# Optimization experiments

Hardware: AMD Instinct MI355X
Metric: run time of the kernel (lower is better)

Reference implementation:

```python
import jax, jax.numpy as jnp
import numpy as np

B, S, D, H = 2, 2048, 1024, 16
HD = D // H          # 64
NREF = HD // 2       # 32 Householder reflections
BLOCK = 128          # flex_attention block granularity
ROPE_BASE = 10000.0


def setup_inputs() -> dict:
    key = jax.random.key(0)
    ks = jax.random.split(key, 12)
    x = jax.random.normal(ks[0], (B, S, D), jnp.float32)
    # block-causal block mask (flex_attention block_mask analogue)
    nb = S // BLOCK
    bm = jnp.tril(jnp.ones((nb, nb), bool))
    mask = jnp.repeat(jnp.repeat(bm, BLOCK, axis=0), BLOCK, axis=1)  # [S,S]
    s = lambda fan: fan ** -0.5
    vs = jax.random.normal(ks[1], (NREF, HD), jnp.float32) * 0.02
    w_qkv = jax.random.normal(ks[2], (D, 3 * D), jnp.float32) * s(D)
    w_out = jax.random.normal(ks[3], (D, D), jnp.float32) * s(D)
    w_gate = jax.random.normal(ks[4], (D, D), jnp.float32) * s(D)
    b_gate = jnp.zeros((D,), jnp.float32)
    w_mlp_gate = jax.random.normal(ks[5], (D, 8 * D), jnp.float32) * s(D)
    b_mlp_gate = jnp.zeros((8 * D,), jnp.float32)
    w_mlp_out = jax.random.normal(ks[6], (4 * D, D), jnp.float32) * s(4 * D)
    b_mlp_out = jnp.zeros((D,), jnp.float32)
    return dict(x=x, mask=mask, grid_size=S, vs=vs, w_qkv=w_qkv, w_out=w_out,
                w_gate=w_gate, b_gate=b_gate, w_mlp_gate=w_mlp_gate,
                b_mlp_gate=b_mlp_gate, w_mlp_out=w_mlp_out, b_mlp_out=b_mlp_out)


def rmsnorm(x):
    return x * jax.lax.rsqrt(jnp.mean(x * x, axis=-1, keepdims=True) + 1e-6)


def householder_matrix(vs):
    # Q = prod_i (I - 2 v_i v_i^T / |v_i|^2), applied sequentially as in torch loop
    def body(Q, v):
        vn = jnp.sum(v * v) + 1e-8
        return Q - (2.0 / vn) * jnp.outer(v, v @ Q), None
    Q0 = jnp.eye(HD, dtype=vs.dtype)
    Q, _ = jax.lax.scan(body, Q0, vs)
    return Q


def rope_tables(seq_len, dtype):
    inv_freq = 1.0 / (ROPE_BASE ** (jnp.arange(0, HD, 2, dtype=jnp.float32) / HD))
    ang = jnp.arange(seq_len, dtype=jnp.float32)[:, None] * inv_freq  # [S, HD/2]
    ang = jnp.concatenate([ang, ang], axis=-1)                        # [S, HD]
    return jnp.cos(ang).astype(dtype), jnp.sin(ang).astype(dtype)


def rotate_half(x):
    x1, x2 = jnp.split(x, 2, axis=-1)
    return jnp.concatenate([-x2, x1], axis=-1)


def reference(x, mask, grid_size, vs, w_qkv, w_out, w_gate, b_gate,
              w_mlp_gate, b_mlp_gate, w_mlp_out, b_mlp_out):
    del grid_size  # positions derived from sequence length
    resid = x
    h = rmsnorm(x)
    qkv = h @ w_qkv                                # [B,S,3D]
    q, k, v = jnp.split(qkv, 3, axis=-1)
    to_heads = lambda t: t.reshape(B, S, H, HD).transpose(0, 2, 1, 3)  # [B,H,S,hd]
    q, k, v = to_heads(q), to_heads(k), to_heads(v)

    # RnRoPE: inverse Householder rotation, rope, forward Householder rotation
    Q = householder_matrix(vs)                     # [hd,hd]
    q = q @ Q.T
    k = k @ Q.T
    cos, sin = rope_tables(S, x.dtype)             # [S,hd]
    cos = cos[None, None]; sin = sin[None, None]
    q = q * cos + rotate_half(q) * sin
    k = k * cos + rotate_half(k) * sin
    q = q @ Q
    k = k @ Q

    # block-sparse attention (mask realized as boolean [S,S])
    scores = jnp.einsum('bhqd,bhkd->bhqk', q, k) / jnp.sqrt(jnp.asarray(HD, x.dtype))
    scores = jnp.where(mask[None, None], scores, jnp.asarray(-1e30, x.dtype))
    attn = jnp.einsum('bhqk,bhkd->bhqd', jax.nn.softmax(scores, axis=-1), v)
    attn = attn.transpose(0, 2, 1, 3).reshape(B, S, D)
    attn = attn @ w_out

    gate = jax.nn.sigmoid(attn @ w_gate + b_gate)
    x = resid + attn * gate

    resid = x
    gv = rmsnorm(x) @ w_mlp_gate + b_mlp_gate      # [B,S,8D]
    g, val = jnp.split(gv, 2, axis=-1)
    x = resid + (val * jax.nn.gelu(g, approximate=False)) @ w_mlp_out + b_mlp_out
    return x
```

## Files before the change

kernel.cpp:

```cpp
#include <hip/hip_runtime.h>
#include <hip/hip_bf16.h>
#include <math.h>

#define BT 2
#define SEQ 2048
#define DIM 1024
#define NH 16
#define HD 64
#define NTOK (BT*SEQ)

typedef __attribute__((ext_vector_type(4))) float floatx4;
typedef __attribute__((ext_vector_type(8))) short shortx8;
typedef __attribute__((ext_vector_type(4))) short shortx4;

#define GLL16(gp, lp) __builtin_amdgcn_global_load_lds( \
    (const __attribute__((address_space(1))) unsigned int*)(const void*)(gp), \
    (__attribute__((address_space(3))) unsigned int*)(void*)(lp), 16, 0, 0)

__device__ __forceinline__ float bf2f(unsigned short u) {
    unsigned int x = ((unsigned int)u) << 16;
    return __builtin_bit_cast(float, x);
}
__device__ __forceinline__ unsigned short f2bf(float f) {
    unsigned int x = __builtin_bit_cast(unsigned int, f);
    unsigned int lsb = (x >> 16) & 1u;
    x += 0x7fffu + lsb;
    return (unsigned short)(x >> 16);
}
__device__ __forceinline__ float ldin_f(const void* p, size_t i, int isbf) {
    return isbf ? bf2f(((const unsigned short*)p)[i]) : ((const float*)p)[i];
}

__global__ void detect_kernel(const unsigned short* __restrict__ x, int* __restrict__ flag) {
    __shared__ int cnt;
    if (threadIdx.x == 0) cnt = 0;
    __syncthreads();
    unsigned short u = x[(size_t)threadIdx.x * 2];
    int e = (u >> 7) & 0xFF;
    if (e >= 100 && e <= 140) atomicAdd(&cnt, 1);
    __syncthreads();
    if (threadIdx.x == 0) *flag = (cnt >= 192) ? 1 : 0;
}

__global__ void transpose_any(const void* __restrict__ in,
                              unsigned short* __restrict__ out, int R, int C,
                              const int* __restrict__ flagp) {
    int isbf = *flagp;
    __shared__ unsigned short tile[32][33];
    int c0 = blockIdx.x * 32, r0 = blockIdx.y * 32;
    int tx = threadIdx.x, ty = threadIdx.y;
#pragma unroll
    for (int i = 0; i < 4; i++) {
        size_t idx = (size_t)(r0 + ty + i * 8) * C + c0 + tx;
        tile[ty + i * 8][tx] = isbf ? ((const unsigned short*)in)[idx]
                                    : f2bf(((const float*)in)[idx]);
    }
    __syncthreads();
#pragma unroll
    for (int i = 0; i < 4; i++)
        out[(size_t)(c0 + ty + i * 8) * R + r0 + tx] = tile[tx][ty + i * 8];
}

__global__ __launch_bounds__(64) void householder_kernel(const void* __restrict__ vs,
                                                         float* __restrict__ Qg,
                                                         const int* __restrict__ flagp) {
    int isbf = *flagp;
    __shared__ float vsh[64];
    int j = threadIdx.x;
    float Qc[64];
#pragma unroll
    for (int i = 0; i < 64; i++) Qc[i] = (i == j) ? 1.f : 0.f;
    for (int r = 0; r < 32; r++) {
        vsh[j] = ldin_f(vs, r * 64 + j, isbf);
        __syncthreads();
        float va[64];
#pragma unroll
        for (int i = 0; i < 64; i++) va[i] = vsh[i];
        float vn0 = 0.f, vn1 = 0.f, vn2 = 0.f, vn3 = 0.f;
        float t0 = 0.f, t1 = 0.f, t2 = 0.f, t3 = 0.f;
#pragma unroll
        for (int i = 0; i < 16; i++) {
            vn0 += va[4 * i + 0] * va[4 * i + 0];
            vn1 += va[4 * i + 1] * va[4 * i + 1];
            vn2 += va[4 * i + 2] * va[4 * i + 2];
            vn3 += va[4 * i + 3] * va[4 * i + 3];
            t0 += va[4 * i + 0] * Qc[4 * i + 0];
            t1 += va[4 * i + 1] * Qc[4 * i + 1];
            t2 += va[4 * i + 2] * Qc[4 * i + 2];
            t3 += va[4 * i + 3] * Qc[4 * i + 3];
        }
        float vn = (vn0 + vn1) + (vn2 + vn3) + 1e-8f;
        float t = (t0 + t1) + (t2 + t3);
        float c = (2.f / vn) * t;
#pragma unroll
        for (int i = 0; i < 64; i++) Qc[i] -= c * va[i];
        __syncthreads();
    }
#pragma unroll
    for (int i = 0; i < 64; i++) Qg[i * 64 + j] = Qc[i];
}

__global__ __launch_bounds__(256) void rotate_wqkv(unsigned short* __restrict__ wT,
                                                   const float* __restrict__ Qg) {
    __shared__ float Qs[64][64];
    __shared__ unsigned short tile[64][128];
    int bid = blockIdx.x;
    int row0 = (bid >> 3) * 64;
    int col0 = (bid & 7) * 128;
    int t = threadIdx.x;
#pragma unroll
    for (int i = 0; i < 16; i++) {
        int idx = i * 256 + t;
        Qs[idx >> 6][idx & 63] = Qg[idx];
    }
#pragma unroll
    for (int i = 0; i < 8; i++) {
        int e = i * 256 + t;
        int r = e >> 5, cg = (e & 31) * 4;
        *(shortx4*)&tile[r][cg] = *(const shortx4*)&wT[(size_t)(row0 + r) * 1024 + col0 + cg];
    }
    __syncthreads();
    int ib = t >> 5;
    int c = (t & 31) * 4;
    float acc[8][4];
#pragma unroll
    for (int rr = 0; rr < 8; rr++)
#pragma unroll
        for (int cx = 0; cx < 4; cx++) acc[rr][cx] = 0.f;
    for (int j = 0; j < 64; j++) {
        float t0 = bf2f(tile[j][c]);
        float t1 = bf2f(tile[j][c + 1]);
        float t2 = bf2f(tile[j][c + 2]);
        float t3 = bf2f(tile[j][c + 3]);
#pragma unroll
        for (int rr = 0; rr < 8; rr++) {
            float qv = Qs[rr * 8 + ib][j];
            acc[rr][0] += qv * t0;
            acc[rr][1] += qv * t1;
            acc[rr][2] += qv * t2;
            acc[rr][3] += qv * t3;
        }
    }
#pragma unroll
    for (int rr = 0; rr < 8; rr++) {
        int i = rr * 8 + ib;
        shortx4 o4;
#pragma unroll
        for (int cx = 0; cx < 4; cx++) o4[cx] = (short)f2bf(acc[rr][cx]);
        *(shortx4*)&wT[(size_t)(row0 + i) * 1024 + col0 + c] = o4;
    }
}

__global__ void rope_table(float* __restrict__ tab) {
    int idx = blockIdx.x * 256 + threadIdx.x;
    int s = idx >> 5, fi = idx & 31;
    float invf = __expf(-(float)fi * (9.210340371976184f / 32.f));
    float ang = (float)s * invf;
    tab[2 * idx]     = cosf(ang);
    tab[2 * idx + 1] = sinf(ang);
}

__global__ __launch_bounds__(256) void rmsnorm2(const void* __restrict__ x,
                                                unsigned short* __restrict__ h,
                                                const int* __restrict__ flagp) {
    int isbf = flagp ? *flagp : 1;
    __shared__ float red[256];
    int row = blockIdx.x, t = threadIdx.x;
    size_t base = (size_t)row * DIM;
    float v[4];
    float ss = 0.f;
#pragma unroll
    for (int i = 0; i < 4; i++) {
        v[i] = ldin_f(x, base + t + 256 * i, isbf);
        ss += v[i] * v[i];
    }
    red[t] = ss;
    __syncthreads();
    for (int s = 128; s > 0; s >>= 1) {
        if (t < s) red[t] += red[t + s];
        __syncthreads();
    }
    float rs = rsqrtf(red[0] * (1.f / 1024.f) + 1e-6f);
#pragma unroll
    for (int i = 0; i < 4; i++) h[base + t + 256 * i] = f2bf(v[i] * rs);
}

template<int BN, int MODE>
__global__ __launch_bounds__(256) void gemm_bt(const unsigned short* __restrict__ A,
                                               const unsigned short* __restrict__ Bt,
                                               void* __restrict__ C,
                                               const void* __restrict__ bias,
                                               const unsigned short* __restrict__ resid,
                                               const void* __restrict__ xin,
                                               const int* __restrict__ flagp,
                                               int M, int N, int K) {
    constexpr int NJ = BN / 32;
    __shared__ __align__(16) unsigned short As[2][128][32];
    __shared__ __align__(16) unsigned short Bs[2][BN][32];
    int isbf = flagp ? *flagp : 1;
    int tile = (blockIdx.x & 7) * (gridDim.x >> 3) + (blockIdx.x >> 3);
    int nbn = N / BN;
    int m0 = (tile / nbn) * 128;
    int n0 = (tile % nbn) * BN;
    int t = threadIdx.x;
    int lane = t & 63;
    int w = t >> 6;
    int wr = (w >> 1) * 64;
    int wc = (w & 1) * (16 * NJ);
    int lr = lane & 15;
    int kg = lane >> 4;

    floatx4 acc[4][NJ];
#pragma unroll
    for (int i = 0; i < 4; i++)
#pragma unroll
        for (int j = 0; j < NJ; j++) acc[i][j] = (floatx4){0.f, 0.f, 0.f, 0.f};

    int srow = w * 16 + (lane >> 2);
    int skseg = (lane & 3) * 8;
    const unsigned short* aP = A + (size_t)(m0 + srow) * K + skseg;
    const unsigned short* bP = Bt + (size_t)(n0 + srow) * K + skseg;
    size_t r64 = (size_t)64 * K;

    auto STAGE = [&](int s, int b) {
        int off = s * 32;
        GLL16(aP + off,       &As[b][w * 16][0]);
        GLL16(aP + r64 + off, &As[b][64 + w * 16][0]);
        GLL16(bP + off,       &Bs[b][w * 16][0]);
        if constexpr (BN == 128) GLL16(bP + r64 + off, &Bs[b][64 + w * 16][0]);
    };

    int NS = K / 32;
    STAGE(0, 0);
    __syncthreads();

    int cur = 0;
    for (int s = 0; s < NS; ++s) {
        if (s + 1 < NS) STAGE(s + 1, cur ^ 1);
        shortx8 af[4], bfv[NJ];
#pragma unroll
        for (int i = 0; i < 4; i++) af[i] = *(const shortx8*)&As[cur][wr + i * 16 + lr][kg * 8];
#pragma unroll
        for (int j = 0; j < NJ; j++) bfv[j] = *(const shortx8*)&Bs[cur][wc + j * 16 + lr][kg * 8];
#pragma unroll
        for (int i = 0; i < 4; i++)
#pragma unroll
            for (int j = 0; j < NJ; j++)
                acc[i][j] = __builtin_amdgcn_mfma_f32_16x16x32_bf16(af[i], bfv[j], acc[i][j], 0, 0, 0);
        __syncthreads();
        cur ^= 1;
    }
#pragma unroll
    for (int i = 0; i < 4; i++) {
#pragma unroll
        for (int j = 0; j < NJ; j++) {
            int col = n0 + wc + j * 16 + lr;
            int rbase = m0 + wr + i * 16 + kg * 4;
            float bv = bias ? ldin_f(bias, col, isbf) : 0.f;
#pragma unroll
            for (int r = 0; r < 4; r++) {
                float val = acc[i][j][r] + bv;
                size_t oidx = (size_t)(rbase + r) * N + col;
                if constexpr (MODE == 0) {
                    ((unsigned short*)C)[oidx] = f2bf(val);
                } else if constexpr (MODE == 1) {
                    ((float*)C)[oidx] = val + bf2f(resid[oidx]);
                } else {
                    float a = bf2f(resid[oidx]);
                    float sg = 1.f / (1.f + __expf(-val));
                    ((unsigned short*)C)[oidx] = f2bf(ldin_f(xin, oidx, isbf) + a * sg);
                }
            }
        }
    }
}

__global__ __launch_bounds__(256) void gemm_glu(const unsigned short* __restrict__ A,
                                                const unsigned short* __restrict__ Bt,
                                                unsigned short* __restrict__ act,
                                                const void* __restrict__ bias,
                                                const int* __restrict__ flagp) {
    __shared__ __align__(16) unsigned short As[2][128][32];
    __shared__ __align__(16) unsigned short Bg[2][64][32];
    __shared__ __align__(16) unsigned short Bv[2][64][32];
    const int K = 1024;
    int isbf = *flagp;
    int tile = (blockIdx.x & 7) * (gridDim.x >> 3) + (blockIdx.x >> 3);
    int m0 = (tile & 31) * 128;
    int n0 = (tile >> 5) * 64;
    int t = threadIdx.x;
    int lane = t & 63;
    int w = t >> 6;
    int wr = (w >> 1) * 64;
    int wc = (w & 1) * 32;
    int lr = lane & 15;
    int kg = lane >> 4;

    floatx4 ag[4][2], av[4][2];
#pragma unroll
    for (int i = 0; i < 4; i++)
#pragma unroll
        for (int j = 0; j < 2; j++) {
            ag[i][j] = (floatx4){0.f, 0.f, 0.f, 0.f};
            av[i][j] = (floatx4){0.f, 0.f, 0.f, 0.f};
        }

    int srow = w * 16 + (lane >> 2);
    int skseg = (lane & 3) * 8;
    const unsigned short* aP  = A + (size_t)(m0 + srow) * K + skseg;
    const unsigned short* bgP = Bt + (size_t)(n0 + srow) * K + skseg;
    const unsigned short* bvP = Bt + (size_t)(4096 + n0 + srow) * K + skseg;
    size_t r64 = (size_t)64 * K;

    auto STAGE = [&](int s, int b) {
        int off = s * 32;
        GLL16(aP + off,       &As[b][w * 16][0]);
        GLL16(aP + r64 + off, &As[b][64 + w * 16][0]);
        GLL16(bgP + off,      &Bg[b][w * 16][0]);
        GLL16(bvP + off,      &Bv[b][w * 16][0]);
    };

    const int NS = K / 32;
    STAGE(0, 0);
    __syncthreads();

    int cur = 0;
    for (int s = 0; s < NS; ++s) {
        if (s + 1 < NS) STAGE(s + 1, cur ^ 1);
        shortx8 af[4], gf[2], vf[2];
#pragma unroll
        for (int i = 0; i < 4; i++) af[i] = *(const shortx8*)&As[cur][wr + i * 16 + lr][kg * 8];
#pragma unroll
        for (int j = 0; j < 2; j++) {
            gf[j] = *(const shortx8*)&Bg[cur][wc + j * 16 + lr][kg * 8];
            vf[j] = *(const shortx8*)&Bv[cur][wc + j * 16 + lr][kg * 8];
        }
#pragma unroll
        for (int i = 0; i < 4; i++)
#pragma unroll
            for (int j = 0; j < 2; j++) {
                ag[i][j] = __builtin_amdgcn_mfma_f32_16x16x32_bf16(af[i], gf[j], ag[i][j], 0, 0, 0);
                av[i][j] = __builtin_amdgcn_mfma_f32_16x16x32_bf16(af[i], vf[j], av[i][j], 0, 0, 0);
            }
        __syncthreads();
        cur ^= 1;
    }
#pragma unroll
    for (int i = 0; i < 4; i++) {
#pragma unroll
        for (int j = 0; j < 2; j++) {
            int col = n0 + wc + j * 16 + lr;
            int rbase = m0 + wr + i * 16 + kg * 4;
            float bgv = ldin_f(bias, col, isbf);
            float bvv = ldin_f(bias, 4096 + col, isbf);
#pragma unroll
            for (int r = 0; r < 4; r++) {
                float g = ag[i][j][r] + bgv;
                float v = av[i][j][r] + bvv;
                float ge = 0.5f * g * (1.f + erff(g * 0.70710678118f));
                act[(size_t)(rbase + r) * 4096 + col] = f2bf(v * ge);
            }
        }
    }
}

__global__ __launch_bounds__(256) void qk_rope3(const unsigned short* __restrict__ qkv,
                                                const float* __restrict__ tab,
                                                unsigned short* __restrict__ q_r,
                                                unsigned short* __restrict__ k_r) {
    int tid = blockIdx.x * 256 + threadIdx.x;
    int c = tid & 3;
    int h = (tid >> 2) & 15;
    int ts = tid >> 6;
    int s = ts & 2047, b = ts >> 11;
    int d0 = c * 8;
    const unsigned short* base = qkv + (size_t)ts * 3072 + h * 64;
    shortx8 qlo = *(const shortx8*)(base + d0);
    shortx8 qhi = *(const shortx8*)(base + d0 + 32);
    shortx8 klo = *(const shortx8*)(base + 1024 + d0);
    shortx8 khi = *(const shortx8*)(base + 1024 + d0 + 32);
    const float* tp = tab + (size_t)s * 64 + d0 * 2;
    shortx8 oql, oqh, okl, okh;
#pragma unroll
    for (int i = 0; i < 8; i++) {
        float cv = tp[2 * i], sv = tp[2 * i + 1];
        float ql = bf2f((unsigned short)qlo[i]), qh = bf2f((unsigned short)qhi[i]);
        float kl = bf2f((unsigned short)klo[i]), kh = bf2f((unsigned short)khi[i]);
        oql[i] = (short)f2bf(ql * cv - qh * sv);
        oqh[i] = (short)f2bf(qh * cv + ql * sv);
        okl[i] = (short)f2bf(kl * cv - kh * sv);
        okh[i] = (short)f2bf(kh * cv + kl * sv);
    }
    size_t o = ((size_t)(b * NH + h) * SEQ + s) * HD + d0;
    *(shortx8*)(q_r + o)      = oql;
    *(shortx8*)(q_r + o + 32) = oqh;
    *(shortx8*)(k_r + o)      = okl;
    *(shortx8*)(k_r + o + 32) = okh;
}

__global__ __launch_bounds__(512) void attn_mfma(const unsigned short* __restrict__ q_r,
                                                 const unsigned short* __restrict__ k_r,
                                                 const unsigned short* __restrict__ qkv,
                                                 unsigned short* __restrict__ attn) {
    __shared__ __align__(16) unsigned short Ks[64][72];
    __shared__ __align__(16) unsigned short Vt[64 * 72];
    __shared__ __align__(16) unsigned short Ps[8][16][72];
    int bid = blockIdx.x;
    int qblk = 15 - (bid & 15);
    int bh = bid >> 4;
    int b = bh >> 4, h = bh & 15;
    size_t bh_off = (size_t)bh * SEQ * HD;
    int tid = threadIdx.x;
    int wv = tid >> 6, lane = tid & 63;
    int l16 = lane & 15, quad = lane >> 4;
    int q0 = qblk * 128 + wv * 16;

    const unsigned short* qrow = q_r + bh_off + (size_t)(q0 + l16) * HD + quad * 8;
    shortx8 aq0 = *(const shortx8*)(qrow);
    shortx8 aq1 = *(const shortx8*)(qrow + 32);

    floatx4 o[4];
#pragma unroll
    for (int nt = 0; nt < 4; nt++) o[nt] = (floatx4){0.f, 0.f, 0.f, 0.f};
    float m_run = -1e30f, l_run = 0.f;

    int nk = (qblk + 1) * 128;
    int skey = tid >> 3;
    int sd0 = (tid & 7) * 8;
    const unsigned short* kbase = k_r + bh_off + (size_t)skey * HD + sd0;
    const unsigned short* vbase = qkv + ((size_t)(b * SEQ + skey)) * 3072 + 2048 + h * 64 + sd0;
    int vco = (((skey >> 3) ^ (tid & 7)) * 8) + (skey & 7);

    shortx8 kv = *(const shortx8*)kbase;
    shortx8 vvv = *(const shortx8*)vbase;

    for (int k0 = 0; k0 < nk; k0 += 64) {
        __syncthreads();
        *(shortx8*)&Ks[skey][sd0] = kv;
#pragma unroll
        for (int i = 0; i < 8; i++) Vt[(size_t)(sd0 + i) * 72 + vco] = (unsigned short)vvv[i];
        __syncthreads();
        if (k0 + 64 < nk) {
            kv  = *(const shortx8*)(kbase + (size_t)(k0 + 64) * HD);
            vvv = *(const shortx8*)(vbase + (size_t)(k0 + 64) * 3072);
        }

        floatx4 sc[4];
#pragma unroll
        for (int kt = 0; kt < 4; kt++) {
            shortx8 bk0 = *(const shortx8*)&Ks[kt * 16 + l16][quad * 8];
            shortx8 bk1 = *(const shortx8*)&Ks[kt * 16 + l16][32 + quad * 8];
            floatx4 z = (floatx4){0.f, 0.f, 0.f, 0.f};
            z = __builtin_amdgcn_mfma_f32_16x16x32_bf16(bk0, aq0, z, 0, 0, 0);
            z = __builtin_amdgcn_mfma_f32_16x16x32_bf16(bk1, aq1, z, 0, 0, 0);
            sc[kt] = z;
        }
        float sv[16], mx[16];
#pragma unroll
        for (int kt = 0; kt < 4; kt++)
#pragma unroll
            for (int r = 0; r < 4; r++) sv[kt * 4 + r] = sc[kt][r] * 0.125f;
#pragma unroll
        for (int i = 0; i < 16; i++) mx[i] = sv[i];
#pragma unroll
        for (int st = 8; st > 0; st >>= 1)
#pragma unroll
            for (int i = 0; i < 8; i++)
                if (i < st) mx[i] = fmaxf(mx[i], mx[i + st]);
        float mt = mx[0];
        mt = fmaxf(mt, __shfl_xor(mt, 16, 64));
        mt = fmaxf(mt, __shfl_xor(mt, 32, 64));
        float nm = fmaxf(m_run, mt);
        float al = __expf(m_run - nm);
        m_run = nm;
        float p[16];
#pragma unroll
        for (int i = 0; i < 16; i++) p[i] = __expf(sv[i] - nm);
        float sm[8];
#pragma unroll
        for (int i = 0; i < 8; i++) sm[i] = p[i] + p[i + 8];
        float ps = ((sm[0] + sm[1]) + (sm[2] + sm[3])) + ((sm[4] + sm[5]) + (sm[6] + sm[7]));
        ps += __shfl_xor(ps, 16, 64);
        ps += __shfl_xor(ps, 32, 64);
        l_run = l_run * al + ps;
#pragma unroll
        for (int kt = 0; kt < 4; kt++) {
            shortx4 pk;
#pragma unroll
            for (int r = 0; r < 4; r++) pk[r] = (short)f2bf(p[kt * 4 + r]);
            *(shortx4*)&Ps[wv][l16][kt * 16 + quad * 4] = pk;
        }
#pragma unroll
        for (int r = 0; r < 4; r++) {
            float alr = __shfl(al, quad * 4 + r, 64);
            o[0][r] *= alr; o[1][r] *= alr; o[2][r] *= alr; o[3][r] *= alr;
        }
#pragma unroll
        for (int h2 = 0; h2 < 2; h2++) {
            shortx8 ap = *(const shortx8*)&Ps[wv][l16][h2 * 32 + quad * 8];
#pragma unroll
            for (int nt = 0; nt < 4; nt++) {
                int dd = nt * 16 + l16;
                shortx8 bvv = *(const shortx8*)&Vt[(size_t)dd * 72 +
                                                   (((h2 * 4 + quad) ^ ((dd >> 3) & 7)) * 8)];
                o[nt] = __builtin_amdgcn_mfma_f32_16x16x32_bf16(ap, bvv, o[nt], 0, 0, 0);
            }
        }
    }
#pragma unroll
    for (int r = 0; r < 4; r++) {
        float lv = __shfl(l_run, quad * 4 + r, 64);
        float inv_l = 1.f / lv;
        int s = q0 + quad * 4 + r;
        unsigned short* op = attn + ((size_t)(b * SEQ + s)) * DIM + h * 64;
#pragma unroll
        for (int nt = 0; nt < 4; nt++) op[nt * 16 + l16] = f2bf(o[nt][r] * inv_l);
    }
}

extern "C" void kernel_launch(void* const* d_in, const int* in_sizes, int n_in,
                              void* d_out, int out_size, void* d_ws, size_t ws_size,
                              hipStream_t stream) {
    const unsigned short* x        = (const unsigned short*)d_in[0];
    const void* vs       = d_in[3];
    const void* w_qkv    = d_in[4];
    const void* w_out    = d_in[5];
    const void* w_gate   = d_in[6];
    const void* b_gate   = d_in[7];
    const void* w_mlp_g  = d_in[8];
    const void* b_mlp_g  = d_in[9];
    const void* w_mlp_o  = d_in[10];
    const void* b_mlp_o  = d_in[11];
    float* out = (float*)d_out;
    char* ws = (char*)d_ws;

    if (n_in < 12) return;
    if (in_sizes[0] != 4194304 || in_sizes[3] != 2048 || in_sizes[4] != 3145728 ||
        in_sizes[8] != 8388608 || in_sizes[10] != 4194304 || in_sizes[7] != 1024) return;

    const size_t o_T   = 0;
    const size_t o_Qg  = 35651584;
    const size_t o_h   = 35684352;
    const size_t o_B   = 44072960;
    const size_t o_C   = 69238784;
    const size_t o_gv  = 94404608;
    const size_t total = 161513472;
    if (ws_size < total) return;

    unsigned short* wqkvT  = (unsigned short*)(ws + o_T);
    unsigned short* woutT  = (unsigned short*)(ws + o_T + 6291456);
    unsigned short* wgateT = (unsigned short*)(ws + o_T + 8388608);
    unsigned short* wmgT   = (unsigned short*)(ws + o_T + 10485760);
    unsigned short* wmoT   = (unsigned short*)(ws + o_T + 27262976);
    float*          Qg     = (float*)(ws + o_Qg);
    int*            flagp  = (int*)(ws + o_Qg + 16384);
    unsigned short* h      = (unsigned short*)(ws + o_h);
    unsigned short* qkv    = (unsigned short*)(ws + o_B);
    unsigned short* ao     = (unsigned short*)(ws + o_B + 8388608);
    unsigned short* q_rb   = (unsigned short*)(ws + o_C);
    unsigned short* k_rb   = (unsigned short*)(ws + o_C + 8388608);
    unsigned short* attnb  = (unsigned short*)(ws + o_C + 16777216);
    unsigned short* x1     = (unsigned short*)(ws + o_C);
    unsigned short* act    = (unsigned short*)(ws + o_C + 8388608);
    float*          rtab   = (float*)(ws + o_gv);

    detect_kernel<<<1, 256, 0, stream>>>(x, flagp);
    householder_kernel<<<1, 64, 0, stream>>>(vs, Qg, flagp);
    rope_table<<<256, 256, 0, stream>>>(rtab);

    dim3 tb(32, 8);
    transpose_any<<<dim3(3072 / 32, 1024 / 32), tb, 0, stream>>>(w_qkv,   wqkvT, 1024, 3072, flagp);
    transpose_any<<<dim3(1024 / 32, 1024 / 32), tb, 0, stream>>>(w_out,   woutT, 1024, 1024, flagp);
    transpose_any<<<dim3(1024 / 32, 1024 / 32), tb, 0, stream>>>(w_gate,  wgateT, 1024, 1024, flagp);
    transpose_any<<<dim3(8192 / 32, 1024 / 32), tb, 0, stream>>>(w_mlp_g, wmgT, 1024, 8192, flagp);
    transpose_any<<<dim3(1024 / 32, 4096 / 32), tb, 0, stream>>>(w_mlp_o, wmoT, 4096, 1024, flagp);
    rotate_wqkv<<<256, 256, 0, stream>>>(wqkvT, Qg);

    rmsnorm2<<<NTOK, 256, 0, stream>>>(x, h, flagp);
    gemm_bt<128, 0><<<32 * 24, 256, 0, stream>>>(h, wqkvT, qkv, nullptr, nullptr, nullptr, flagp, NTOK, 3072, 1024);
    qk_rope3<<<1024, 256, 0, stream>>>(qkv, rtab, q_rb, k_rb);
    attn_mfma<<<BT * NH * (SEQ / 128), 512, 0, stream>>>(q_rb, k_rb, qkv, attnb);
    gemm_bt<64, 0><<<32 * 16, 256, 0, stream>>>(attnb, woutT, ao, nullptr, nullptr, nullptr, flagp, NTOK, 1024, 1024);
    gemm_bt<64, 2><<<32 * 16, 256, 0, stream>>>(ao, wgateT, x1, b_gate, ao, x, flagp, NTOK, 1024, 1024);
    rmsnorm2<<<NTOK, 256, 0, stream>>>(x1, h, nullptr);
    gemm_glu<<<32 * 64, 256, 0, stream>>>(h, wmgT, act, b_mlp_g, flagp);
    gemm_bt<64, 1><<<32 * 16, 256, 0, stream>>>(act, wmoT, (void*)out, b_mlp_o, x1, nullptr, flagp, NTOK, 1024, 4096);
}
```

Baseline: 562.4 us.

## Triple-buffer GEMM LDS staging with explicit vmcnt waits instead of full syncthreads

Both the generic bt GEMM and the GLU GEMM move from double to triple-buffered LDS tiles, prefetching two K-steps ahead. The per-iteration __syncthreads is replaced by a partial vmcnt wait that keeps the newest stage in flight, followed by an lgkmcnt wait and a raw barrier. The aim is to hide global-to-LDS load latency behind the MFMA work. The cost is 50% more shared memory per block, which may lower occupancy. Correctness depends on the hand-written vmcnt counts matching the number of loads issued per stage.

New measurement: 570.5 us. About the same (+1.5%).

```diff
diff --git a/kernel.cpp b/kernel.cpp
--- a/kernel.cpp
+++ b/kernel.cpp
@@ -16,6 +16,17 @@
 #define GLL16(gp, lp) __builtin_amdgcn_global_load_lds( \
     (const __attribute__((address_space(1))) unsigned int*)(const void*)(gp), \
     (__attribute__((address_space(3))) unsigned int*)(void*)(lp), 16, 0, 0)
+
+template<int N> __device__ __forceinline__ void waitvm() {
+    if constexpr (N == 0) asm volatile("s_waitcnt vmcnt(0)" ::: "memory");
+    else if constexpr (N == 3) asm volatile("s_waitcnt vmcnt(3)" ::: "memory");
+    else if constexpr (N == 4) asm volatile("s_waitcnt vmcnt(4)" ::: "memory");
+}
+__device__ __forceinline__ void barrier_lgkm() {
+    asm volatile("s_waitcnt lgkmcnt(0)" ::: "memory");
+    __builtin_amdgcn_s_barrier();
+    asm volatile("" ::: "memory");
+}
 
 __device__ __forceinline__ float bf2f(unsigned short u) {
     unsigned int x = ((unsigned int)u) << 16;
@@ -195,8 +206,9 @@
                                                const int* __restrict__ flagp,
                                                int M, int N, int K) {
     constexpr int NJ = BN / 32;
-    __shared__ __align__(16) unsigned short As[2][128][32];
-    __shared__ __align__(16) unsigned short Bs[2][BN][32];
+    constexpr int NLD = (BN == 128) ? 4 : 3;
+    __shared__ __align__(16) unsigned short As[3][128][32];
+    __shared__ __align__(16) unsigned short Bs[3][BN][32];
     int isbf = flagp ? *flagp : 1;
     int tile = (blockIdx.x & 7) * (gridDim.x >> 3) + (blockIdx.x >> 3);
     int nbn = N / BN;
@@ -232,23 +244,28 @@
 
     int NS = K / 32;
     STAGE(0, 0);
-    __syncthreads();
-
-    int cur = 0;
+    STAGE(1, 1);
+    waitvm<NLD>();
+    barrier_lgkm();
+
+    int cb = 0, sb = 2;
     for (int s = 0; s < NS; ++s) {
-        if (s + 1 < NS) STAGE(s + 1, cur ^ 1);
+        if (s + 2 < NS) STAGE(s + 2, sb);
         shortx8 af[4], bfv[NJ];
 #pragma unroll
-        for (int i = 0; i < 4; i++) af[i] = *(const shortx8*)&As[cur][wr + i * 16 + lr][kg * 8];
-#pragma unroll
-        for (int j = 0; j < NJ; j++) bfv[j] = *(const shortx8*)&Bs[cur][wc + j * 16 + lr][kg * 8];
+        for (int i = 0; i < 4; i++) af[i] = *(const shortx8*)&As[cb][wr + i * 16 + lr][kg * 8];
+#pragma unroll
+        for (int j = 0; j < NJ; j++) bfv[j] = *(const shortx8*)&Bs[cb][wc + j * 16 + lr][kg * 8];
 #pragma unroll
         for (int i = 0; i < 4; i++)
 #pragma unroll
             for (int j = 0; j < NJ; j++)
                 acc[i][j] = __builtin_amdgcn_mfma_f32_16x16x32_bf16(af[i], bfv[j], acc[i][j], 0, 0, 0);
-        __syncthreads();
-        cur ^= 1;
+        if (s + 2 < NS)      waitvm<NLD>();
+        else if (s + 1 < NS) waitvm<0>();
+        barrier_lgkm();
+        cb = (cb == 2) ? 0 : cb + 1;
+        sb = (sb == 2) ? 0 : sb + 1;
     }
 #pragma unroll
     for (int i = 0; i < 4; i++) {
@@ -280,9 +297,9 @@
                                                 unsigned short* __restrict__ act,
                                                 const void* __restrict__ bias,
                                                 const int* __restrict__ flagp) {
-    __shared__ __align__(16) unsigned short As[2][128][32];
-    __shared__ __align__(16) unsigned short Bg[2][64][32];
-    __shared__ __align__(16) unsigned short Bv[2][64][32];
+    __shared__ __align__(16) unsigned short As[3][128][32];
+    __shared__ __align__(16) unsigned short Bg[3][64][32];
+    __shared__ __align__(16) unsigned short Bv[3][64][32];
     const int K = 1024;
     int isbf = *flagp;
     int tile = (blockIdx.x & 7) * (gridDim.x >> 3) + (blockIdx.x >> 3);
@@ -322,18 +339,20 @@
 
     const int NS = K / 32;
     STAGE(0, 0);
-    __syncthreads();
-
-    int cur = 0;
+    STAGE(1, 1);
+    waitvm<4>();
+    barrier_lgkm();
+
+    int cb = 0, sb = 2;
     for (int s = 0; s < NS; ++s) {
-        if (s + 1 < NS) STAGE(s + 1, cur ^ 1);
+        if (s + 2 < NS) STAGE(s + 2, sb);
         shortx8 af[4], gf[2], vf[2];
 #pragma unroll
-        for (int i = 0; i < 4; i++) af[i] = *(const shortx8*)&As[cur][wr + i * 16 + lr][kg * 8];
+        for (int i = 0; i < 4; i++) af[i] = *(const shortx8*)&As[cb][wr + i * 16 + lr][kg * 8];
 #pragma unroll
         for (int j = 0; j < 2; j++) {
-            gf[j] = *(const shortx8*)&Bg[cur][wc + j * 16 + lr][kg * 8];
-            vf[j] = *(const shortx8*)&Bv[cur][wc + j * 16 + lr][kg * 8];
+            gf[j] = *(const shortx8*)&Bg[cb][wc + j * 16 + lr][kg * 8];
+            vf[j] = *(const shortx8*)&Bv[cb][wc + j * 16 + lr][kg * 8];
         }
 #pragma unroll
         for (int i = 0; i < 4; i++)
@@ -342,8 +361,11 @@
                 ag[i][j] = __builtin_amdgcn_mfma_f32_16x16x32_bf16(af[i], gf[j], ag[i][j], 0, 0, 0);
                 av[i][j] = __builtin_amdgcn_mfma_f32_16x16x32_bf16(af[i], vf[j], av[i][j], 0, 0, 0);
             }
-        __syncthreads();
-        cur ^= 1;
+        if (s + 2 < NS)      waitvm<4>();
+        else if (s + 1 < NS) waitvm<0>();
+        barrier_lgkm();
+        cb = (cb == 2) ? 0 : cb + 1;
+        sb = (sb == 2) ? 0 : sb + 1;
     }
 #pragma unroll
     for (int i = 0; i < 4; i++) {
```

## Deepen GEMM K-tile to 64 with XOR-swizzled LDS and unrolled double buffer

Applied to the files above, without the earlier changes.

Both GEMM kernels now stage 64-wide K slices instead of 32, halving the number of barrier-separated iterations. Global-to-LDS loads place 16-byte segments at XOR-swizzled positions so the later fragment reads avoid LDS bank conflicts. The double-buffer loop is unrolled by two with fixed buffer indices. The QKV projection drops its 128-wide N tile and uses 64-wide tiles with twice as many blocks. LDS per block doubles, which may lower occupancy.

Measured after the change: 541.4 us. 1.04x faster.

```diff
diff --git a/kernel.cpp b/kernel.cpp
--- a/kernel.cpp
+++ b/kernel.cpp
@@ -185,7 +185,7 @@
     for (int i = 0; i < 4; i++) h[base + t + 256 * i] = f2bf(v[i] * rs);
 }
 
-template<int BN, int MODE>
+template<int MODE>
 __global__ __launch_bounds__(256) void gemm_bt(const unsigned short* __restrict__ A,
                                                const unsigned short* __restrict__ Bt,
                                                void* __restrict__ C,
@@ -194,73 +194,93 @@
                                                const void* __restrict__ xin,
                                                const int* __restrict__ flagp,
                                                int M, int N, int K) {
-    constexpr int NJ = BN / 32;
-    __shared__ __align__(16) unsigned short As[2][128][32];
-    __shared__ __align__(16) unsigned short Bs[2][BN][32];
+    __shared__ __align__(16) unsigned short As[2][128][64];
+    __shared__ __align__(16) unsigned short Bs[2][64][64];
     int isbf = flagp ? *flagp : 1;
     int tile = (blockIdx.x & 7) * (gridDim.x >> 3) + (blockIdx.x >> 3);
-    int nbn = N / BN;
+    int nbn = N >> 6;
     int m0 = (tile / nbn) * 128;
-    int n0 = (tile % nbn) * BN;
+    int n0 = (tile % nbn) * 64;
     int t = threadIdx.x;
     int lane = t & 63;
     int w = t >> 6;
     int wr = (w >> 1) * 64;
-    int wc = (w & 1) * (16 * NJ);
+    int wc = (w & 1) * 32;
     int lr = lane & 15;
     int kg = lane >> 4;
-
-    floatx4 acc[4][NJ];
+    int l8 = lane >> 3, s8 = lane & 7;
+    int segswz = (s8 ^ l8) * 8;
+    int cs0 = ((kg)     ^ (lr & 7)) * 8;
+    int cs1 = ((4 + kg) ^ (lr & 7)) * 8;
+
+    floatx4 acc[4][2];
 #pragma unroll
     for (int i = 0; i < 4; i++)
 #pragma unroll
-        for (int j = 0; j < NJ; j++) acc[i][j] = (floatx4){0.f, 0.f, 0.f, 0.f};
-
-    int srow = w * 16 + (lane >> 2);
-    int skseg = (lane & 3) * 8;
-    const unsigned short* aP = A + (size_t)(m0 + srow) * K + skseg;
-    const unsigned short* bP = Bt + (size_t)(n0 + srow) * K + skseg;
-    size_t r64 = (size_t)64 * K;
-
-    auto STAGE = [&](int s, int b) {
-        int off = s * 32;
-        GLL16(aP + off,       &As[b][w * 16][0]);
-        GLL16(aP + r64 + off, &As[b][64 + w * 16][0]);
-        GLL16(bP + off,       &Bs[b][w * 16][0]);
-        if constexpr (BN == 128) GLL16(bP + r64 + off, &Bs[b][64 + w * 16][0]);
+        for (int j = 0; j < 2; j++) acc[i][j] = (floatx4){0.f, 0.f, 0.f, 0.f};
+
+    int rbase = w * 8 + l8;
+    const unsigned short* aP0 = A + (size_t)(m0 + rbase +  0) * K + segswz;
+    const unsigned short* aP1 = A + (size_t)(m0 + rbase + 32) * K + segswz;
+    const unsigned short* aP2 = A + (size_t)(m0 + rbase + 64) * K + segswz;
+    const unsigned short* aP3 = A + (size_t)(m0 + rbase + 96) * K + segswz;
+    const unsigned short* bP0 = Bt + (size_t)(n0 + rbase +  0) * K + segswz;
+    const unsigned short* bP1 = Bt + (size_t)(n0 + rbase + 32) * K + segswz;
+
+    auto STAGE = [&](int s, int B) {
+        int off = s * 64;
+        GLL16(aP0 + off, &As[B][w * 8 +  0][0]);
+        GLL16(aP1 + off, &As[B][w * 8 + 32][0]);
+        GLL16(aP2 + off, &As[B][w * 8 + 64][0]);
+        GLL16(aP3 + off, &As[B][w * 8 + 96][0]);
+        GLL16(bP0 + off, &Bs[B][w * 8 +  0][0]);
+        GLL16(bP1 + off, &Bs[B][w * 8 + 32][0]);
     };
-
-    int NS = K / 32;
+    auto MM = [&](int B) {
+        shortx8 af[4][2], bf[2][2];
+#pragma unroll
+        for (int i = 0; i < 4; i++) {
+            af[i][0] = *(const shortx8*)&As[B][wr + i * 16 + lr][cs0];
+            af[i][1] = *(const shortx8*)&As[B][wr + i * 16 + lr][cs1];
+        }
+#pragma unroll
+        for (int j = 0; j < 2; j++) {
+            bf[j][0] = *(const shortx8*)&Bs[B][wc + j * 16 + lr][cs0];
+            bf[j][1] = *(const shortx8*)&Bs[B][wc + j * 16 + lr][cs1];
+        }
+#pragma unroll
+        for (int i = 0; i < 4; i++)
+#pragma unroll
+            for (int j = 0; j < 2; j++) {
+                acc[i][j] = __builtin_amdgcn_mfma_f32_16x16x32_bf16(af[i][0], bf[j][0], acc[i][j], 0, 0, 0);
+                acc[i][j] = __builtin_amdgcn_mfma_f32_16x16x32_bf16(af[i][1], bf[j][1], acc[i][j], 0, 0, 0);
+            }
+    };
+
+    int NS = K >> 6;
     STAGE(0, 0);
     __syncthreads();
-
-    int cur = 0;
-    for (int s = 0; s < NS; ++s) {
-        if (s + 1 < NS) STAGE(s + 1, cur ^ 1);
-        shortx8 af[4], bfv[NJ];
-#pragma unroll
-        for (int i = 0; i < 4; i++) af[i] = *(const shortx8*)&As[cur][wr + i * 16 + lr][kg * 8];
-#pragma unroll
-        for (int j = 0; j < NJ; j++) bfv[j] = *(const shortx8*)&Bs[cur][wc + j * 16 + lr][kg * 8];
-#pragma unroll
-        for (int i = 0; i < 4; i++)
-#pragma unroll
-            for (int j = 0; j < NJ; j++)
-                acc[i][j] = __builtin_amdgcn_mfma_f32_16x16x32_bf16(af[i], bfv[j], acc[i][j], 0, 0, 0);
+    for (int s = 0; s < NS; s += 2) {
+        if (s + 1 < NS) STAGE(s + 1, 1);
+        MM(0);
         __syncthreads();
-        cur ^= 1;
+        if (s + 1 < NS) {
+            if (s + 2 < NS) STAGE(s + 2, 0);
+            MM(1);
+            __syncthreads();
+        }
     }
 #pragma unroll
     for (int i = 0; i < 4; i++) {
 #pragma unroll
-        for (int j = 0; j < NJ; j++) {
+        for (int j = 0; j < 2; j++) {
             int col = n0 + wc + j * 16 + lr;
-            int rbase = m0 + wr + i * 16 + kg * 4;
+            int rb = m0 + wr + i * 16 + kg * 4;
             float bv = bias ? ldin_f(bias, col, isbf) : 0.f;
 #pragma unroll
             for (int r = 0; r < 4; r++) {
                 float val = acc[i][j][r] + bv;
-                size_t oidx = (size_t)(rbase + r) * N + col;
+                size_t oidx = (size_t)(rb + r) * N + col;
                 if constexpr (MODE == 0) {
                     ((unsigned short*)C)[oidx] = f2bf(val);
                 } else if constexpr (MODE == 1) {
@@ -280,9 +300,9 @@
                                                 unsigned short* __restrict__ act,
                                                 const void* __restrict__ bias,
                                                 const int* __restrict__ flagp) {
-    __shared__ __align__(16) unsigned short As[2][128][32];
-    __shared__ __align__(16) unsigned short Bg[2][64][32];
-    __shared__ __align__(16) unsigned short Bv[2][64][32];
+    __shared__ __align__(16) unsigned short As[2][128][64];
+    __shared__ __align__(16) unsigned short Bg[2][64][64];
+    __shared__ __align__(16) unsigned short Bv[2][64][64];
     const int K = 1024;
     int isbf = *flagp;
     int tile = (blockIdx.x & 7) * (gridDim.x >> 3) + (blockIdx.x >> 3);
@@ -295,6 +315,10 @@
     int wc = (w & 1) * 32;
     int lr = lane & 15;
     int kg = lane >> 4;
+    int l8 = lane >> 3, s8 = lane & 7;
+    int segswz = (s8 ^ l8) * 8;
+    int cs0 = ((kg)     ^ (lr & 7)) * 8;
+    int cs1 = ((4 + kg) ^ (lr & 7)) * 8;
 
     floatx4 ag[4][2], av[4][2];
 #pragma unroll
@@ -305,52 +329,71 @@
             av[i][j] = (floatx4){0.f, 0.f, 0.f, 0.f};
         }
 
-    int srow = w * 16 + (lane >> 2);
-    int skseg = (lane & 3) * 8;
-    const unsigned short* aP  = A + (size_t)(m0 + srow) * K + skseg;
-    const unsigned short* bgP = Bt + (size_t)(n0 + srow) * K + skseg;
-    const unsigned short* bvP = Bt + (size_t)(4096 + n0 + srow) * K + skseg;
-    size_t r64 = (size_t)64 * K;
-
-    auto STAGE = [&](int s, int b) {
-        int off = s * 32;
-        GLL16(aP + off,       &As[b][w * 16][0]);
-        GLL16(aP + r64 + off, &As[b][64 + w * 16][0]);
-        GLL16(bgP + off,      &Bg[b][w * 16][0]);
-        GLL16(bvP + off,      &Bv[b][w * 16][0]);
+    int rbase = w * 8 + l8;
+    const unsigned short* aP0 = A + (size_t)(m0 + rbase +  0) * K + segswz;
+    const unsigned short* aP1 = A + (size_t)(m0 + rbase + 32) * K + segswz;
+    const unsigned short* aP2 = A + (size_t)(m0 + rbase + 64) * K + segswz;
+    const unsigned short* aP3 = A + (size_t)(m0 + rbase + 96) * K + segswz;
+    const unsigned short* gP0 = Bt + (size_t)(n0 + rbase +  0) * K + segswz;
+    const unsigned short* gP1 = Bt + (size_t)(n0 + rbase + 32) * K + segswz;
+    const unsigned short* vP0 = Bt + (size_t)(4096 + n0 + rbase +  0) * K + segswz;
+    const unsigned short* vP1 = Bt + (size_t)(4096 + n0 + rbase + 32) * K + segswz;
+
+    auto STAGE = [&](int s, int B) {
+        int off = s * 64;
+        GLL16(aP0 + off, &As[B][w * 8 +  0][0]);
+        GLL16(aP1 + off, &As[B][w * 8 + 32][0]);
+        GLL16(aP2 + off, &As[B][w * 8 + 64][0]);
+        GLL16(aP3 + off, &As[B][w * 8 + 96][0]);
+        GLL16(gP0 + off, &Bg[B][w * 8 +  0][0]);
+        GLL16(gP1 + off, &Bg[B][w * 8 + 32][0]);
+        GLL16(vP0 + off, &Bv[B][w * 8 +  0][0]);
+        GLL16(vP1 + off, &Bv[B][w * 8 + 32][0]);
     };
-
-    const int NS = K / 32;
+    auto MM = [&](int B) {
+        shortx8 af[4][2], gf[2][2], vf[2][2];
+#pragma unroll
+        for (int i = 0; i < 4; i++) {
+            af[i][0] = *(const shortx8*)&As[B][wr + i * 16 + lr][cs0];
+            af[i][1] = *(const shortx8*)&As[B][wr + i * 16 + lr][cs1];
+        }
+#pragma unroll
+        for (int j = 0; j < 2; j++) {
+            gf[j][0] = *(const shortx8*)&Bg[B][wc + j * 16 + lr][cs0];
+            gf[j][1] = *(const shortx8*)&Bg[B][wc + j * 16 + lr][cs1];
+            vf[j][0] = *(const shortx8*)&Bv[B][wc + j * 16 + lr][cs0];
+            vf[j][1] = *(const shortx8*)&Bv[B][wc + j * 16 + lr][cs1];
+        }
+#pragma unroll
+        for (int i = 0; i < 4; i++)
+#pragma unroll
+            for (int j = 0; j < 2; j++) {
+                ag[i][j] = __builtin_amdgcn_mfma_f32_16x16x32_bf16(af[i][0], gf[j][0], ag[i][j], 0, 0, 0);
+                ag[i][j] = __builtin_amdgcn_mfma_f32_16x16x32_bf16(af[i][1], gf[j][1], ag[i][j], 0, 0, 0);
+                av[i][j] = __builtin_amdgcn_mfma_f32_16x16x32_bf16(af[i][0], vf[j][0], av[i][j], 0, 0, 0);
+                av[i][j] = __builtin_amdgcn_mfma_f32_16x16x32_bf16(af[i][1], vf[j][1], av[i][j], 0, 0, 0);
+            }
+    };
+
+    const int NS = K >> 6;
     STAGE(0, 0);
     __syncthreads();
-
-    int cur = 0;
-    for (int s = 0; s < NS; ++s) {
-        if (s + 1 < NS) STAGE(s + 1, cur ^ 1);
-        shortx8 af[4], gf[2], vf[2];
-#pragma unroll
-        for (int i = 0; i < 4; i++) af[i] = *(const shortx8*)&As[cur][wr + i * 16 + lr][kg * 8];
-#pragma unroll
-        for (int j = 0; j < 2; j++) {
-            gf[j] = *(const shortx8*)&Bg[cur][wc + j * 16 + lr][kg * 8];
-            vf[j] = *(const shortx8*)&Bv[cur][wc + j * 16 + lr][kg * 8];
-        }
-#pragma unroll
-        for (int i = 0; i < 4; i++)
-#pragma unroll
-            for (int j = 0; j < 2; j++) {
-                ag[i][j] = __builtin_amdgcn_mfma_f32_16x16x32_bf16(af[i], gf[j], ag[i][j], 0, 0, 0);
-                av[i][j] = __builtin_amdgcn_mfma_f32_16x16x32_bf16(af[i], vf[j], av[i][j], 0, 0, 0);
-            }
+    for (int s = 0; s < NS; s += 2) {
+        if (s + 1 < NS) STAGE(s + 1, 1);
+        MM(0);
         __syncthreads();
-        cur ^= 1;
+        if (s + 1 < NS) {
+            if (s + 2 < NS) STAGE(s + 2, 0);
+            MM(1);
+            __syncthreads();
+        }
     }
 #pragma unroll
     for (int i = 0; i < 4; i++) {
 #pragma unroll
         for (int j = 0; j < 2; j++) {
             int col = n0 + wc + j * 16 + lr;
-            int rbase = m0 + wr + i * 16 + kg * 4;
+            int rb = m0 + wr + i * 16 + kg * 4;
             float bgv = ldin_f(bias, col, isbf);
             float bvv = ldin_f(bias, 4096 + col, isbf);
 #pragma unroll
@@ -358,7 +401,7 @@
                 float g = ag[i][j][r] + bgv;
                 float v = av[i][j][r] + bvv;
                 float ge = 0.5f * g * (1.f + erff(g * 0.70710678118f));
-                act[(size_t)(rbase + r) * 4096 + col] = f2bf(v * ge);
+                act[(size_t)(rb + r) * 4096 + col] = f2bf(v * ge);
             }
         }
     }
@@ -577,12 +620,12 @@
     rotate_wqkv<<<256, 256, 0, stream>>>(wqkvT, Qg);
 
     rmsnorm2<<<NTOK, 256, 0, stream>>>(x, h, flagp);
-    gemm_bt<128, 0><<<32 * 24, 256, 0, stream>>>(h, wqkvT, qkv, nullptr, nullptr, nullptr, flagp, NTOK, 3072, 1024);
+    gemm_bt<0><<<32 * 48, 256, 0, stream>>>(h, wqkvT, qkv, nullptr, nullptr, nullptr, flagp, NTOK, 3072, 1024);
     qk_rope3<<<1024, 256, 0, stream>>>(qkv, rtab, q_rb, k_rb);
     attn_mfma<<<BT * NH * (SEQ / 128), 512, 0, stream>>>(q_rb, k_rb, qkv, attnb);
-    gemm_bt<64, 0><<<32 * 16, 256, 0, stream>>>(attnb, woutT, ao, nullptr, nullptr, nullptr, flagp, NTOK, 1024, 1024);
-    gemm_bt<64, 2><<<32 * 16, 256, 0, stream>>>(ao, wgateT, x1, b_gate, ao, x, flagp, NTOK, 1024, 1024);
+    gemm_bt<0><<<32 * 16, 256, 0, stream>>>(attnb, woutT, ao, nullptr, nullptr, nullptr, flagp, NTOK, 1024, 1024);
+    gemm_bt<2><<<32 * 16, 256, 0, stream>>>(ao, wgateT, x1, b_gate, ao, x, flagp, NTOK, 1024, 1024);
     rmsnorm2<<<NTOK, 256, 0, stream>>>(x1, h, nullptr);
     gemm_glu<<<32 * 64, 256, 0, stream>>>(h, wmgT, act, b_mlp_g, flagp);
-    gemm_bt<64, 1><<<32 * 16, 256, 0, stream>>>(act, wmoT, (void*)out, b_mlp_o, x1, nullptr, flagp, NTOK, 1024, 4096);
-}
+    gemm_bt<1><<<32 * 16, 256, 0, stream>>>(act, wmoT, (void*)out, b_mlp_o, x1, nullptr, flagp, NTOK, 1024, 4096);
+}
```
